# Optimization experiments

Hardware: AMD Instinct MI355X
Metric: run time of the kernel (lower is better)

Reference implementation:

```python
import jax, jax.numpy as jnp
import numpy as np

B, IN_DIM, D, C = 16384, 1024, 256, 100


def setup_inputs() -> dict:
    key = jax.random.key(0)
    k1, k2, k3, k4 = jax.random.split(key, 4)
    x = jax.random.normal(k1, (B, IN_DIM), dtype=jnp.float32)
    W = jax.random.normal(k2, (IN_DIM, D), dtype=jnp.float32) * (1.0 / np.sqrt(IN_DIM))
    b = jax.random.normal(k3, (D,), dtype=jnp.float32) * 0.01
    P = jax.random.normal(k4, (C, D), dtype=jnp.float32)  # class prototypes [C, D]
    return {"x": x, "W": W, "b": b, "P": P}


def reference(x, W, b, P):
    # Encoder: Z = x @ W + b  -> [B, D]
    Z = x @ W + b
    d = Z.shape[-1]
    # MSE(r, p) = mean((r - p)^2) = (|r|^2 - 2 r.p + |p|^2) / D
    # Computed via expansion to avoid the [B, C, D] broadcast intermediate.
    sq = (
        jnp.sum(Z * Z, axis=-1, keepdims=True)      # [B, 1]
        - 2.0 * (Z @ P.T)                            # [B, C]
        + jnp.sum(P * P, axis=-1)[None, :]           # [1, C]
    )
    return -sq / d  # [B, C]
```

## Files before the change

kernel.cpp:

```cpp
#include <hip/hip_runtime.h>

#define BATCH 16384
#define KDIM  1024
#define DDIM  256
#define CNUM  100
#define CPAD  112

typedef __bf16 bf16x4 __attribute__((ext_vector_type(4)));
typedef __bf16 bf16x8 __attribute__((ext_vector_type(8)));
typedef float  floatx4 __attribute__((ext_vector_type(4)));

static __device__ __forceinline__ unsigned short f2b(float f) {
    return __builtin_bit_cast(unsigned short, (__bf16)f);
}

static __device__ __forceinline__ void gload_lds16(const unsigned short* g,
                                                   unsigned short* l) {
    __builtin_amdgcn_global_load_lds(
        (const __attribute__((address_space(1))) unsigned int*)g,
        (__attribute__((address_space(3))) unsigned int*)l, 16, 0, 0);
}

__global__ __launch_bounds__(256) void prep(const float* __restrict__ W,
                                            const float* __restrict__ P,
                                            unsigned short* __restrict__ Wt,
                                            unsigned short* __restrict__ Pbf,
                                            float* __restrict__ pnorm2) {
    __shared__ float T[32][33];
    const int bid = blockIdx.x;
    if (bid < 256) {
        const int k0 = (bid & 31) * 32;
        const int n0 = (bid >> 5) * 32;
        const int j  = threadIdx.x & 31;
        const int i0 = threadIdx.x >> 5;
#pragma unroll
        for (int l = 0; l < 4; ++l) {
            int i = i0 + l * 8;
            T[i][j] = W[(k0 + i) * DDIM + n0 + j];
        }
        __syncthreads();
#pragma unroll
        for (int l = 0; l < 4; ++l) {
            int i = i0 + l * 8;
            Wt[(n0 + i) * KDIM + k0 + j] = f2b(T[j][i]);
        }
    } else {
        const int wave = threadIdx.x >> 6;
        const int lane = threadIdx.x & 63;
        const int c = (bid - 256) * 4 + wave;
        float s = 0.f;
#pragma unroll
        for (int jj = 0; jj < 4; ++jj) {
            int d = jj * 64 + lane;
            float v = (c < CNUM) ? P[c * DDIM + d] : 0.f;
            Pbf[c * DDIM + d] = f2b(v);
            s += v * v;
        }
#pragma unroll
        for (int m = 1; m < 64; m <<= 1) s += __shfl_xor(s, m, 64);
        if (lane == 0) pnorm2[c] = s;
    }
}

__global__ __launch_bounds__(256, 2) void fused_main(
    const float* __restrict__ x, const float* __restrict__ bias,
    const unsigned short* __restrict__ Wt, const unsigned short* __restrict__ Pbf,
    const float* __restrict__ pnorm2, float* __restrict__ out)
{
    __shared__ unsigned short U[36864];
    unsigned short* Zs = U;
    __shared__ float rn2[4][32];

    const int tid  = threadIdx.x;
    const int wave = tid >> 6;
    const int lane = tid & 63;
    const int lm   = lane & 15;
    const int lq   = lane >> 4;
    const int r0   = blockIdx.x * 32;

    const int rowA = tid >> 3;
    const int kbA  = tid & 7;
    const float* gA = x + (r0 + rowA) * KDIM + kbA * 8;
    const int ldsA = rowA * 64 + ((kbA ^ (rowA & 7)) * 8);

    const int gkb = (lane & 7) ^ ((lane >> 3) & 7);
    const unsigned short* gB = Wt + (wave * 64 + (lane >> 3)) * KDIM + gkb * 8;

    const int sw0 = ((0 * 4 + lq) ^ (lm & 7)) * 8;
    const int sw1 = ((1 * 4 + lq) ^ (lm & 7)) * 8;

    floatx4 acc[2][4];
#pragma unroll
    for (int g = 0; g < 2; ++g)
#pragma unroll
        for (int f = 0; f < 4; ++f) { acc[g][f][0]=0.f; acc[g][f][1]=0.f; acc[g][f][2]=0.f; acc[g][f][3]=0.f; }

    {
        floatx4 q0 = *(const floatx4*)(gA);
        floatx4 q1 = *(const floatx4*)(gA + 4);
#pragma unroll
        for (int j = 0; j < 8; ++j)
            gload_lds16(gB + j * 8 * KDIM, U + 4096 + (wave * 64 + j * 8) * 64);
        bf16x8 ha;
        ha[0] = (__bf16)q0[0]; ha[1] = (__bf16)q0[1];
        ha[2] = (__bf16)q0[2]; ha[3] = (__bf16)q0[3];
        ha[4] = (__bf16)q1[0]; ha[5] = (__bf16)q1[1];
        ha[6] = (__bf16)q1[2]; ha[7] = (__bf16)q1[3];
        *(bf16x8*)&U[ldsA] = ha;
    }
    floatx4 pa0 = *(const floatx4*)(gA + 64);
    floatx4 pa1 = *(const floatx4*)(gA + 68);
    __syncthreads();

#pragma unroll 2
    for (int kk = 0; kk < KDIM; kk += 64) {
        const int cur = (kk >> 6) & 1;
        const int nxt = cur ^ 1;
        unsigned short* As_c = U + cur * 2048;
        unsigned short* Bs_c = U + 4096 + cur * 16384;
        if (kk + 64 < KDIM) {
            unsigned short* Bs_n = U + 4096 + nxt * 16384;
#pragma unroll
            for (int j = 0; j < 8; ++j)
                gload_lds16(gB + j * 8 * KDIM + kk + 64, Bs_n + (wave * 64 + j * 8) * 64);
            bf16x8 ha;
            ha[0] = (__bf16)pa0[0]; ha[1] = (__bf16)pa0[1];
            ha[2] = (__bf16)pa0[2]; ha[3] = (__bf16)pa0[3];
            ha[4] = (__bf16)pa1[0]; ha[5] = (__bf16)pa1[1];
            ha[6] = (__bf16)pa1[2]; ha[7] = (__bf16)pa1[3];
            *(bf16x8*)&(U + nxt * 2048)[ldsA] = ha;
            if (kk + 128 < KDIM) {
                pa0 = *(const floatx4*)(gA + kk + 128);
                pa1 = *(const floatx4*)(gA + kk + 132);
            }
        }
#pragma unroll
        for (int kf = 0; kf < 2; ++kf) {
            const int sw = kf ? sw1 : sw0;
            bf16x8 a0 = *(const bf16x8*)&As_c[lm * 64 + sw];
            bf16x8 a1 = *(const bf16x8*)&As_c[(16 + lm) * 64 + sw];
#pragma unroll
            for (int f = 0; f < 4; ++f) {
                bf16x8 bfr = *(const bf16x8*)&Bs_c[(wave * 64 + f * 16 + lm) * 64 + sw];
                acc[0][f] = __builtin_amdgcn_mfma_f32_16x16x32_bf16(a0, bfr, acc[0][f], 0, 0, 0);
                acc[1][f] = __builtin_amdgcn_mfma_f32_16x16x32_bf16(a1, bfr, acc[1][f], 0, 0, 0);
            }
        }
        __syncthreads();
    }

#pragma unroll
    for (int f = 0; f < 4; ++f) {
        float bb = bias[wave * 64 + f * 16 + lm];
#pragma unroll
        for (int g = 0; g < 2; ++g)
#pragma unroll
            for (int r = 0; r < 4; ++r) acc[g][f][r] += bb;
    }

#pragma unroll
    for (int g = 0; g < 2; ++g) {
        float s0 = 0.f, s1 = 0.f, s2 = 0.f, s3 = 0.f;
#pragma unroll
        for (int f = 0; f < 4; ++f) {
            s0 += acc[g][f][0] * acc[g][f][0];
            s1 += acc[g][f][1] * acc[g][f][1];
            s2 += acc[g][f][2] * acc[g][f][2];
            s3 += acc[g][f][3] * acc[g][f][3];
        }
#pragma unroll
        for (int m = 1; m < 16; m <<= 1) {
            s0 += __shfl_xor(s0, m, 64);
            s1 += __shfl_xor(s1, m, 64);
            s2 += __shfl_xor(s2, m, 64);
            s3 += __shfl_xor(s3, m, 64);
        }
        if (lm == 0) {
            int rl = g * 16 + lq * 4;
            rn2[wave][rl + 0] = s0;
            rn2[wave][rl + 1] = s1;
            rn2[wave][rl + 2] = s2;
            rn2[wave][rl + 3] = s3;
        }
    }

#pragma unroll
    for (int g = 0; g < 2; ++g)
#pragma unroll
        for (int f = 0; f < 4; ++f) {
            int col = wave * 64 + f * 16 + lm;
#pragma unroll
            for (int r = 0; r < 4; ++r)
                Zs[(g * 16 + lq * 4 + r) * 264 + col] = f2b(acc[g][f][r]);
        }
    __syncthreads();

#pragma unroll
    for (int t = 0; t < 2; ++t) {
        const int ct = wave * 2 + t;
        if (ct < 7) {
            floatx4 acc2[2];
#pragma unroll
            for (int nf = 0; nf < 2; ++nf) { acc2[nf][0]=0.f; acc2[nf][1]=0.f; acc2[nf][2]=0.f; acc2[nf][3]=0.f; }
            const unsigned short* gP = Pbf + (ct * 16 + lm) * DDIM + lq * 8;
#pragma unroll
            for (int ks = 0; ks < 8; ++ks) {
                bf16x8 ap = *(const bf16x8*)(gP + ks * 32);
#pragma unroll
                for (int nf = 0; nf < 2; ++nf) {
                    bf16x8 bz = *(const bf16x8*)&Zs[(nf * 16 + lm) * 264 + ks * 32 + lq * 8];
                    acc2[nf] = __builtin_amdgcn_mfma_f32_16x16x32_bf16(ap, bz, acc2[nf], 0, 0, 0);
                }
            }
            int c0 = ct * 16 + lq * 4;
            if (c0 < CNUM) {
                floatx4 pn = *(const floatx4*)(pnorm2 + c0);
#pragma unroll
                for (int nf = 0; nf < 2; ++nf) {
                    int rl = nf * 16 + lm;
                    float rn = rn2[0][rl] + rn2[1][rl] + rn2[2][rl] + rn2[3][rl];
                    floatx4 o;
#pragma unroll
                    for (int r = 0; r < 4; ++r)
                        o[r] = (2.f * acc2[nf][r] - rn - pn[r]) * (1.f / 256.f);
                    *(floatx4*)&out[(r0 + rl) * CNUM + c0] = o;
                }
            }
        }
    }
}

extern "C" void kernel_launch(void* const* d_in, const int* in_sizes, int n_in,
                              void* d_out, int out_size, void* d_ws, size_t ws_size,
                              hipStream_t stream) {
    const float* x = (const float*)d_in[0];
    const float* W = (const float*)d_in[1];
    const float* b = (const float*)d_in[2];
    const float* P = (const float*)d_in[3];
    float* out = (float*)d_out;

    unsigned short* Wt  = (unsigned short*)d_ws;
    unsigned short* Pbf = Wt + KDIM * DDIM;
    float* pn2 = (float*)(Pbf + CPAD * DDIM);

    prep<<<256 + CPAD / 4, 256, 0, stream>>>(W, P, Wt, Pbf, pn2);
    fused_main<<<BATCH / 32, 256, 0, stream>>>(x, b, Wt, Pbf, pn2, out);
}
```

Measured before the change: 116.3 us.

## Double block row tile to 64 with 8 waves and finer LDS waits

Each block now handles 64 rows with 512 threads arranged as a 2x4 wave grid, so every W tile staged in LDS is reused across twice as many rows and the grid is halved. The full __syncthreads in the K loop becomes an explicit vmcnt wait plus s_barrier, letting the prefetched x registers stay in flight across the barrier. The second GEMM against the prototypes now runs on 7 waves, each covering 64 rows. In exchange the block uses about 115 KB of LDS, which permits only one block per CU even though launch bounds still ask for two, and the hand-coded waitcnt immediates are fragile.

After: 116.8 us. No clear change (+0.5%).

```diff
diff --git a/kernel.cpp b/kernel.cpp
--- a/kernel.cpp
+++ b/kernel.cpp
@@ -62,21 +62,26 @@
     }
 }
 
-__global__ __launch_bounds__(256, 2) void fused_main(
+__global__ __launch_bounds__(512, 2) void fused_main(
     const float* __restrict__ x, const float* __restrict__ bias,
     const unsigned short* __restrict__ Wt, const unsigned short* __restrict__ Pbf,
     const float* __restrict__ pnorm2, float* __restrict__ out)
 {
-    __shared__ unsigned short U[36864];
-    unsigned short* Zs = U;
-    __shared__ float rn2[4][32];
+    __shared__ unsigned short As0[64 * 64];
+    __shared__ unsigned short As1[64 * 64];
+    __shared__ unsigned short Bs0[256 * 64];
+    __shared__ unsigned short Bs1[256 * 64];
+    __shared__ unsigned short Zs[64 * 264];
+    __shared__ float rn2[4][64];
 
     const int tid  = threadIdx.x;
     const int wave = tid >> 6;
     const int lane = tid & 63;
     const int lm   = lane & 15;
     const int lq   = lane >> 4;
-    const int r0   = blockIdx.x * 32;
+    const int rc   = wave & 1;
+    const int cc   = wave >> 1;
+    const int r0   = blockIdx.x * 64;
 
     const int rowA = tid >> 3;
     const int kbA  = tid & 7;
@@ -84,7 +89,8 @@
     const int ldsA = rowA * 64 + ((kbA ^ (rowA & 7)) * 8);
 
     const int gkb = (lane & 7) ^ ((lane >> 3) & 7);
-    const unsigned short* gB = Wt + (wave * 64 + (lane >> 3)) * KDIM + gkb * 8;
+    const unsigned short* gB = Wt + (wave * 32 + (lane >> 3)) * KDIM + gkb * 8;
+    const int ldsBoff = wave * 32 * 64;
 
     const int sw0 = ((0 * 4 + lq) ^ (lm & 7)) * 8;
     const int sw1 = ((1 * 4 + lq) ^ (lm & 7)) * 8;
@@ -99,59 +105,65 @@
         floatx4 q0 = *(const floatx4*)(gA);
         floatx4 q1 = *(const floatx4*)(gA + 4);
 #pragma unroll
-        for (int j = 0; j < 8; ++j)
-            gload_lds16(gB + j * 8 * KDIM, U + 4096 + (wave * 64 + j * 8) * 64);
+        for (int j = 0; j < 4; ++j)
+            gload_lds16(gB + j * 8 * KDIM, Bs0 + ldsBoff + j * 8 * 64);
         bf16x8 ha;
         ha[0] = (__bf16)q0[0]; ha[1] = (__bf16)q0[1];
         ha[2] = (__bf16)q0[2]; ha[3] = (__bf16)q0[3];
         ha[4] = (__bf16)q1[0]; ha[5] = (__bf16)q1[1];
         ha[6] = (__bf16)q1[2]; ha[7] = (__bf16)q1[3];
-        *(bf16x8*)&U[ldsA] = ha;
+        *(bf16x8*)&As0[ldsA] = ha;
     }
     floatx4 pa0 = *(const floatx4*)(gA + 64);
     floatx4 pa1 = *(const floatx4*)(gA + 68);
-    __syncthreads();
-
-#pragma unroll 2
-    for (int kk = 0; kk < KDIM; kk += 64) {
-        const int cur = (kk >> 6) & 1;
-        const int nxt = cur ^ 1;
-        unsigned short* As_c = U + cur * 2048;
-        unsigned short* Bs_c = U + 4096 + cur * 16384;
+    __builtin_amdgcn_s_waitcnt(0x0072);
+    __builtin_amdgcn_s_barrier();
+
+#pragma unroll
+    for (int it = 0; it < 16; ++it) {
+        const int kk = it * 64;
+        unsigned short* As_c = (it & 1) ? As1 : As0;
+        unsigned short* Bs_c = (it & 1) ? Bs1 : Bs0;
+        unsigned short* As_n = (it & 1) ? As0 : As1;
+        unsigned short* Bs_n = (it & 1) ? Bs0 : Bs1;
+
         if (kk + 64 < KDIM) {
-            unsigned short* Bs_n = U + 4096 + nxt * 16384;
-#pragma unroll
-            for (int j = 0; j < 8; ++j)
-                gload_lds16(gB + j * 8 * KDIM + kk + 64, Bs_n + (wave * 64 + j * 8) * 64);
+#pragma unroll
+            for (int j = 0; j < 4; ++j)
+                gload_lds16(gB + j * 8 * KDIM + kk + 64, Bs_n + ldsBoff + j * 8 * 64);
             bf16x8 ha;
             ha[0] = (__bf16)pa0[0]; ha[1] = (__bf16)pa0[1];
             ha[2] = (__bf16)pa0[2]; ha[3] = (__bf16)pa0[3];
             ha[4] = (__bf16)pa1[0]; ha[5] = (__bf16)pa1[1];
             ha[6] = (__bf16)pa1[2]; ha[7] = (__bf16)pa1[3];
-            *(bf16x8*)&(U + nxt * 2048)[ldsA] = ha;
+            *(bf16x8*)&As_n[ldsA] = ha;
             if (kk + 128 < KDIM) {
                 pa0 = *(const floatx4*)(gA + kk + 128);
                 pa1 = *(const floatx4*)(gA + kk + 132);
             }
         }
+
 #pragma unroll
         for (int kf = 0; kf < 2; ++kf) {
             const int sw = kf ? sw1 : sw0;
-            bf16x8 a0 = *(const bf16x8*)&As_c[lm * 64 + sw];
-            bf16x8 a1 = *(const bf16x8*)&As_c[(16 + lm) * 64 + sw];
+            bf16x8 a0 = *(const bf16x8*)&As_c[(rc * 32 + lm) * 64 + sw];
+            bf16x8 a1 = *(const bf16x8*)&As_c[(rc * 32 + 16 + lm) * 64 + sw];
 #pragma unroll
             for (int f = 0; f < 4; ++f) {
-                bf16x8 bfr = *(const bf16x8*)&Bs_c[(wave * 64 + f * 16 + lm) * 64 + sw];
+                bf16x8 bfr = *(const bf16x8*)&Bs_c[(cc * 64 + f * 16 + lm) * 64 + sw];
                 acc[0][f] = __builtin_amdgcn_mfma_f32_16x16x32_bf16(a0, bfr, acc[0][f], 0, 0, 0);
                 acc[1][f] = __builtin_amdgcn_mfma_f32_16x16x32_bf16(a1, bfr, acc[1][f], 0, 0, 0);
             }
         }
-        __syncthreads();
+
+        if (kk + 128 < KDIM) __builtin_amdgcn_s_waitcnt(0x0072);
+        else                 __builtin_amdgcn_s_waitcnt(0x0070);
+        __builtin_amdgcn_s_barrier();
     }
 
 #pragma unroll
     for (int f = 0; f < 4; ++f) {
-        float bb = bias[wave * 64 + f * 16 + lm];
+        float bb = bias[cc * 64 + f * 16 + lm];
 #pragma unroll
         for (int g = 0; g < 2; ++g)
 #pragma unroll
@@ -176,11 +188,11 @@
             s3 += __shfl_xor(s3, m, 64);
         }
         if (lm == 0) {
-            int rl = g * 16 + lq * 4;
-            rn2[wave][rl + 0] = s0;
-            rn2[wave][rl + 1] = s1;
-            rn2[wave][rl + 2] = s2;
-            rn2[wave][rl + 3] = s3;
+            int rl = rc * 32 + g * 16 + lq * 4;
+            rn2[cc][rl + 0] = s0;
+            rn2[cc][rl + 1] = s1;
+            rn2[cc][rl + 2] = s2;
+            rn2[cc][rl + 3] = s3;
         }
     }
 
@@ -188,43 +200,39 @@
     for (int g = 0; g < 2; ++g)
 #pragma unroll
         for (int f = 0; f < 4; ++f) {
-            int col = wave * 64 + f * 16 + lm;
+            int col = cc * 64 + f * 16 + lm;
 #pragma unroll
             for (int r = 0; r < 4; ++r)
-                Zs[(g * 16 + lq * 4 + r) * 264 + col] = f2b(acc[g][f][r]);
+                Zs[(rc * 32 + g * 16 + lq * 4 + r) * 264 + col] = f2b(acc[g][f][r]);
         }
     __syncthreads();
 
-#pragma unroll
-    for (int t = 0; t < 2; ++t) {
-        const int ct = wave * 2 + t;
-        if (ct < 7) {
-            floatx4 acc2[2];
-#pragma unroll
-            for (int nf = 0; nf < 2; ++nf) { acc2[nf][0]=0.f; acc2[nf][1]=0.f; acc2[nf][2]=0.f; acc2[nf][3]=0.f; }
-            const unsigned short* gP = Pbf + (ct * 16 + lm) * DDIM + lq * 8;
-#pragma unroll
-            for (int ks = 0; ks < 8; ++ks) {
-                bf16x8 ap = *(const bf16x8*)(gP + ks * 32);
-#pragma unroll
-                for (int nf = 0; nf < 2; ++nf) {
-                    bf16x8 bz = *(const bf16x8*)&Zs[(nf * 16 + lm) * 264 + ks * 32 + lq * 8];
-                    acc2[nf] = __builtin_amdgcn_mfma_f32_16x16x32_bf16(ap, bz, acc2[nf], 0, 0, 0);
-                }
-            }
-            int c0 = ct * 16 + lq * 4;
-            if (c0 < CNUM) {
-                floatx4 pn = *(const floatx4*)(pnorm2 + c0);
-#pragma unroll
-                for (int nf = 0; nf < 2; ++nf) {
-                    int rl = nf * 16 + lm;
-                    float rn = rn2[0][rl] + rn2[1][rl] + rn2[2][rl] + rn2[3][rl];
-                    floatx4 o;
-#pragma unroll
-                    for (int r = 0; r < 4; ++r)
-                        o[r] = (2.f * acc2[nf][r] - rn - pn[r]) * (1.f / 256.f);
-                    *(floatx4*)&out[(r0 + rl) * CNUM + c0] = o;
-                }
+    if (wave < 7) {
+        floatx4 acc2[4];
+#pragma unroll
+        for (int nf = 0; nf < 4; ++nf) { acc2[nf][0]=0.f; acc2[nf][1]=0.f; acc2[nf][2]=0.f; acc2[nf][3]=0.f; }
+        const unsigned short* gP = Pbf + (wave * 16 + lm) * DDIM + lq * 8;
+#pragma unroll
+        for (int ks = 0; ks < 8; ++ks) {
+            bf16x8 ap = *(const bf16x8*)(gP + ks * 32);
+#pragma unroll
+            for (int nf = 0; nf < 4; ++nf) {
+                bf16x8 bz = *(const bf16x8*)&Zs[(nf * 16 + lm) * 264 + ks * 32 + lq * 8];
+                acc2[nf] = __builtin_amdgcn_mfma_f32_16x16x32_bf16(ap, bz, acc2[nf], 0, 0, 0);
+            }
+        }
+        int c0 = wave * 16 + lq * 4;
+        if (c0 < CNUM) {
+            floatx4 pn = *(const floatx4*)(pnorm2 + c0);
+#pragma unroll
+            for (int nf = 0; nf < 4; ++nf) {
+                int rl = nf * 16 + lm;
+                float rn = rn2[0][rl] + rn2[1][rl] + rn2[2][rl] + rn2[3][rl];
+                floatx4 o;
+#pragma unroll
+                for (int r = 0; r < 4; ++r)
+                    o[r] = (2.f * acc2[nf][r] - rn - pn[r]) * (1.f / 256.f);
+                *(floatx4*)&out[(r0 + rl) * CNUM + c0] = o;
             }
         }
     }
@@ -244,5 +252,5 @@
     float* pn2 = (float*)(Pbf + CPAD * DDIM);
 
     prep<<<256 + CPAD / 4, 256, 0, stream>>>(W, P, Wt, Pbf, pn2);
-    fused_main<<<BATCH / 32, 256, 0, stream>>>(x, b, Wt, Pbf, pn2, out);
-}
+    fused_main<<<BATCH / 64, 512, 0, stream>>>(x, b, Wt, Pbf, pn2, out);
+}
```
